# Performance work log

Measured on AMD Instinct MI355X. Metric: run time of the kernel, lower is better.

Reference implementation:

```python
import jax, jax.numpy as jnp
import numpy as np

B, N, D = 32, 2048, 512

def setup_inputs() -> dict:
    key = jax.random.key(0)
    k1, k2, k3, k4 = jax.random.split(key, 4)
    return {
        "src": jax.random.normal(k1, (B, N, 3), dtype=jnp.float32),
        "tgt": jax.random.normal(k2, (B, N, 3), dtype=jnp.float32),
        "src_embed": jax.random.normal(k3, (B, N, D), dtype=jnp.float32),
        "tgt_embed": jax.random.normal(k4, (B, N, D), dtype=jnp.float32),
    }

def reference(src, tgt, src_embed, tgt_embed):
    # src, tgt: (B, N, 3); src_embed, tgt_embed: (B, N, D)
    d_k = jnp.asarray(src_embed.shape[-1], dtype=src_embed.dtype)
    # attention scores (B, N_src, N_tgt), softmax over tgt points
    scores = jnp.einsum('bnd,bmd->bnm', src_embed, tgt_embed) / jnp.sqrt(d_k)
    pointer = jax.nn.softmax(scores, axis=2)
    # matched = tgt^T @ pointer^T -> (B, 3, N_src)
    matched = jnp.einsum('bmc,bnm->bcn', tgt, pointer)
    src_t = jnp.transpose(src, (0, 2, 1))  # (B, 3, N)
    src_cent = jnp.mean(src_t, axis=2, keepdims=True)        # (B, 3, 1)
    matched_cent = jnp.mean(matched, axis=2, keepdims=True)  # (B, 3, 1)
    src_demean = src_t - src_cent
    matched_demean = matched - matched_cent
    # cross-covariance H: (B, 3, 3)
    H = jnp.einsum('bcn,bdn->bcd', src_demean, matched_demean)
    U, _, Vh = jnp.linalg.svd(H, full_matrices=False)  # square 3x3: reduced == full
    V = jnp.transpose(Vh, (0, 2, 1))
    R = jnp.matmul(V, jnp.transpose(U, (0, 2, 1)))
    det = jnp.linalg.det(R)
    identity = jnp.eye(3, dtype=R.dtype)
    reflect = jnp.diag(jnp.array([1.0, 1.0, -1.0], dtype=R.dtype))
    refl = jnp.where((det >= 0)[:, None, None], identity, reflect)
    R = jnp.matmul(refl, R)
    t = jnp.matmul(-R, src_cent) + matched_cent  # (B, 3, 1)
    t = jnp.transpose(t, (0, 2, 1))              # (B, 1, 3)
    return (R, t)
```

## Files before the change

### kernel.cpp

```cpp
#include <hip/hip_runtime.h>
#include <hip/hip_fp16.h>
#include <math.h>

#define B_ 32
#define N_ 2048
#define D_ 512
#define NT 256

typedef __attribute__((ext_vector_type(8))) _Float16 f16x8;
typedef __attribute__((ext_vector_type(8))) short s16x8;
typedef __attribute__((ext_vector_type(4))) float f32x4;
typedef __attribute__((ext_vector_type(4))) unsigned int u32x4;

__device__ inline unsigned packh2(float lo, float hi) {
    __half l = __float2half_rn(lo), h = __float2half_rn(hi);
    return (unsigned)__half_as_ushort(l) | ((unsigned)__half_as_ushort(h) << 16);
}
__device__ inline unsigned f2bf(float x) {
    unsigned u = __float_as_uint(x);
    return (u + 0x7FFFu + ((u >> 16) & 1u)) >> 16;
}
__device__ inline float bf2f(unsigned h) { return __uint_as_float(h << 16); }

__global__ __launch_bounds__(256) void prepass_kernel(
    const float* __restrict__ te, u32x4* __restrict__ kp)
{
    const int idx = blockIdx.x * 256 + threadIdx.x;
    const int b   = idx >> 17;
    const int r17 = idx & 131071;
    const int mt  = r17 >> 13;
    const int kt  = (r17 >> 9) & 15;
    const int o16 = r17 & 511;
    const int r   = o16 >> 2;
    const int s   = o16 & 3;
    const int lg  = s ^ ((r >> 1) & 3);
    const float* src = te + (((size_t)b * N_ + mt * 128 + r) * D_ + kt * 32 + lg * 8);
    const float4 f0 = *(const float4*)src;
    const float4 f1 = *(const float4*)(src + 4);
    u32x4 u;
    u[0] = packh2(f0.x, f0.y);
    u[1] = packh2(f0.z, f0.w);
    u[2] = packh2(f1.x, f1.y);
    u[3] = packh2(f1.z, f1.w);
    kp[idx] = u;
}

__global__ __launch_bounds__(NT, 2) void attn_pipe_kernel(
    const float* __restrict__ src, const float* __restrict__ tgt,
    const float* __restrict__ src_embed, const u32x4* __restrict__ kp,
    float* __restrict__ partials)
{
    __shared__ f16x8 ring[4][512];
    __shared__ float4 Ts4[N_];
    __shared__ double red[4][15];

    const int tid  = threadIdx.x;
    const int wv   = tid >> 6;
    const int lane = tid & 63;
    const int lr   = lane & 15;
    const int lg   = lane >> 4;
    const int sxb  = (lg ^ ((lr >> 1) & 3)) << 4;
    char* ringB = (char*)&ring[0][0];

    const int xcd  = blockIdx.x & 7;
    const int idx  = blockIdx.x >> 3;
    const int b    = xcd * 4 + (idx >> 4);
    const int msl  = idx & 15;
    const int n0   = msl * 128;
    const int pblk = b * 16 + msl;

    const float QSC = 0.044194173824159216f * 1.4426950408889634f;
    f16x8 Qr[2][16];
#pragma unroll
    for (int qf = 0; qf < 2; ++qf) {
        const int qrow = n0 + wv * 32 + qf * 16 + lr;
        const float* qp = src_embed + ((size_t)b * N_ + qrow) * D_ + lg * 8;
#pragma unroll
        for (int s = 0; s < 16; ++s) {
            const float4 f0 = *(const float4*)(qp + s * 32);
            const float4 f1 = *(const float4*)(qp + s * 32 + 4);
            u32x4 u;
            u[0] = packh2(f0.x * QSC, f0.y * QSC);
            u[1] = packh2(f0.z * QSC, f0.w * QSC);
            u[2] = packh2(f1.x * QSC, f1.y * QSC);
            u[3] = packh2(f1.z * QSC, f1.w * QSC);
            Qr[qf][s] = __builtin_bit_cast(f16x8, u);
        }
    }
    {
        const float* tb = tgt + (size_t)b * N_ * 3;
#pragma unroll
        for (int i = 0; i < 8; ++i) {
            const int r = tid + i * 256;
            Ts4[r] = make_float4(tb[r * 3], tb[r * 3 + 1], tb[r * 3 + 2], 0.f);
        }
    }
    __syncthreads();

#define STAGE(mc_, kt_, slot_) do {                                            \
    const u32x4* _g = kp + ((((size_t)b * 16 + (mc_)) * 16 + (kt_)) << 9);     \
    __builtin_amdgcn_global_load_lds(                                          \
        (const __attribute__((address_space(1))) void*)(_g + tid),             \
        (__attribute__((address_space(3))) void*)(&ring[slot_][wv * 64]),      \
        16, 0, 0);                                                             \
    __builtin_amdgcn_global_load_lds(                                          \
        (const __attribute__((address_space(1))) void*)(_g + 256 + tid),       \
        (__attribute__((address_space(3))) void*)(&ring[slot_][256 + wv * 64]),\
        16, 0, 0);                                                             \
} while (0)

    STAGE(0, 0, 0);
    STAGE(0, 1, 1);
    STAGE(0, 2, 2);

    float m_s[2] = {-1e30f, -1e30f}, l_s[2] = {0.f, 0.f};
    float axs[2] = {0.f, 0.f}, ays[2] = {0.f, 0.f}, azs[2] = {0.f, 0.f};

    for (int mc = 0; mc < 16; ++mc) {
        f32x4 acc0[8], acc1[8];
#pragma unroll
        for (int nf = 0; nf < 8; ++nf) {
            acc0[nf] = (f32x4){0.f, 0.f, 0.f, 0.f};
            acc1[nf] = (f32x4){0.f, 0.f, 0.f, 0.f};
        }

#pragma unroll
        for (int kt = 0; kt < 16; ++kt) {
            const int t = (mc << 4) + kt;
            if (mc == 15 && kt >= 14) {
                asm volatile("s_waitcnt vmcnt(0)" ::: "memory");
            } else {
                asm volatile("s_waitcnt vmcnt(4)" ::: "memory");
            }
            __builtin_amdgcn_s_barrier();
            if (t <= 252) {
                const int tn = t + 3;
                STAGE(tn >> 4, tn & 15, tn & 3);
            }
            const char* abase = ringB + ((t & 3) << 13) + lr * 64 + sxb;
#pragma unroll
            for (int nf = 0; nf < 8; ++nf) {
                const f16x8 a = *(const f16x8*)(abase + nf * 1024);
                acc0[nf] = __builtin_amdgcn_mfma_f32_16x16x32_f16(a, Qr[0][kt], acc0[nf], 0, 0, 0);
                acc1[nf] = __builtin_amdgcn_mfma_f32_16x16x32_f16(a, Qr[1][kt], acc1[nf], 0, 0, 0);
            }
        }

        const float4* Ts = &Ts4[mc * 128];
        float mx0 = -1e30f, mx1 = -1e30f;
#pragma unroll
        for (int nf = 0; nf < 8; ++nf)
#pragma unroll
            for (int r4 = 0; r4 < 4; ++r4) {
                mx0 = fmaxf(mx0, acc0[nf][r4]);
                mx1 = fmaxf(mx1, acc1[nf][r4]);
            }
        mx0 = fmaxf(mx0, __shfl_xor(mx0, 16)); mx0 = fmaxf(mx0, __shfl_xor(mx0, 32));
        mx1 = fmaxf(mx1, __shfl_xor(mx1, 16)); mx1 = fmaxf(mx1, __shfl_xor(mx1, 32));
        const float mn0 = fmaxf(m_s[0], mx0), mn1 = fmaxf(m_s[1], mx1);
        const float c0 = exp2f(m_s[0] - mn0), c1 = exp2f(m_s[1] - mn1);
        l_s[0] *= c0; axs[0] *= c0; ays[0] *= c0; azs[0] *= c0; m_s[0] = mn0;
        l_s[1] *= c1; axs[1] *= c1; ays[1] *= c1; azs[1] *= c1; m_s[1] = mn1;
        float l0 = 0.f, x0 = 0.f, y0 = 0.f, z0 = 0.f;
        float l1 = 0.f, x1 = 0.f, y1 = 0.f, z1 = 0.f;
#pragma unroll
        for (int nf = 0; nf < 8; ++nf)
#pragma unroll
            for (int r4 = 0; r4 < 4; ++r4) {
                const float4 tv = Ts[nf * 16 + lg * 4 + r4];
                const float p0 = exp2f(acc0[nf][r4] - mn0);
                const float p1 = exp2f(acc1[nf][r4] - mn1);
                l0 += p0; x0 = fmaf(p0, tv.x, x0); y0 = fmaf(p0, tv.y, y0); z0 = fmaf(p0, tv.z, z0);
                l1 += p1; x1 = fmaf(p1, tv.x, x1); y1 = fmaf(p1, tv.y, y1); z1 = fmaf(p1, tv.z, z1);
            }
        l_s[0] += l0; axs[0] += x0; ays[0] += y0; azs[0] += z0;
        l_s[1] += l1; axs[1] += x1; ays[1] += y1; azs[1] += z1;
    }
#undef STAGE

    double dl[15];
#pragma unroll
    for (int i = 0; i < 15; ++i) dl[i] = 0.0;
#pragma unroll
    for (int qf = 0; qf < 2; ++qf) {
        float lt = l_s[qf], x = axs[qf], y = ays[qf], z = azs[qf];
        lt += __shfl_xor(lt, 16); lt += __shfl_xor(lt, 32);
        x  += __shfl_xor(x, 16);  x  += __shfl_xor(x, 32);
        y  += __shfl_xor(y, 16);  y  += __shfl_xor(y, 32);
        z  += __shfl_xor(z, 16);  z  += __shfl_xor(z, 32);
        if (lg == 0) {
            const int qrow = n0 + wv * 32 + qf * 16 + lr;
            const float* sp = src + ((size_t)b * N_ + qrow) * 3;
            const double inv = 1.0 / (double)lt;
            const double m0d = (double)x * inv, m1d = (double)y * inv, m2d = (double)z * inv;
            const double s0 = sp[0], s1 = sp[1], s2 = sp[2];
            dl[0] += s0;  dl[1] += s1;  dl[2] += s2;
            dl[3] += m0d; dl[4] += m1d; dl[5] += m2d;
            dl[6]  += s0 * m0d; dl[7]  += s0 * m1d; dl[8]  += s0 * m2d;
            dl[9]  += s1 * m0d; dl[10] += s1 * m1d; dl[11] += s1 * m2d;
            dl[12] += s2 * m0d; dl[13] += s2 * m1d; dl[14] += s2 * m2d;
        }
    }
#pragma unroll
    for (int i = 0; i < 15; ++i) {
        double v = dl[i];
        for (int off = 1; off < 64; off <<= 1) v += __shfl_xor(v, off);
        dl[i] = v;
    }
    if (lane == 0) {
#pragma unroll
        for (int i = 0; i < 15; ++i) red[wv][i] = dl[i];
    }
    __syncthreads();
    if (tid < 15) {
        double sum = 0.0;
        for (int w = 0; w < 4; ++w) sum += red[w][tid];
        partials[(size_t)pblk * 15 + tid] = (float)sum;
    }
}

__global__ __launch_bounds__(256, 2) void attn_v2_kernel(
    const float* __restrict__ src, const float* __restrict__ tgt,
    const float* __restrict__ src_embed, const float* __restrict__ tgt_embed,
    float* __restrict__ partials)
{
    __shared__ short Khi_s[128 * 64];
    __shared__ short Klo_s[128 * 64];
    __shared__ float4 Ts4[128];
    __shared__ double red[64][15];

    char* KhiB = (char*)Khi_s;
    char* KloB = (char*)Klo_s;

    const int w    = blockIdx.x;
    const int xcd  = w & 7;
    const int idx  = w >> 3;
    const int b    = xcd * 4 + (idx >> 5);
    const int n0   = (idx & 31) * 64;
    const int blk  = b * 32 + (idx & 31);

    const int tid  = threadIdx.x;
    const int wv   = tid >> 6;
    const int lane = tid & 63;
    const int lr   = lane & 15;
    const int lg   = lane >> 4;
    const unsigned swl = (unsigned)((lr & 7) << 4);

    const float scale = 0.044194173824159216f;
    const float* kbase = tgt_embed + (size_t)b * N_ * D_;

    const int qrow = n0 + wv * 16 + lr;
    const float* qp = src_embed + ((size_t)b * N_ + qrow) * D_ + lg * 8;
    s16x8 qhi[16], qlo[16];
#pragma unroll
    for (int s = 0; s < 16; ++s) {
        const float4 f0 = *reinterpret_cast<const float4*>(qp + s * 32);
        const float4 f1 = *reinterpret_cast<const float4*>(qp + s * 32 + 4);
        const float x[8] = {f0.x, f0.y, f0.z, f0.w, f1.x, f1.y, f1.z, f1.w};
#pragma unroll
        for (int i = 0; i < 8; ++i) {
            const float v = x[i] * scale;
            const unsigned h = f2bf(v);
            qhi[s][i] = (short)h;
            qlo[s][i] = (short)f2bf(v - bf2f(h));
        }
    }

    float m_run = -1e30f, l_run = 0.f, a0 = 0.f, a1 = 0.f, a2 = 0.f;
    const int srow = tid >> 1;
    const int shalf = tid & 1;
    const unsigned swr = (unsigned)((srow & 7) << 4);

    for (int m0 = 0; m0 < N_; m0 += 128) {
        f32x4 acc[8];
#pragma unroll
        for (int nf = 0; nf < 8; ++nf) acc[nf] = (f32x4){0.f, 0.f, 0.f, 0.f};

#pragma unroll
        for (int kt = 0; kt < 8; ++kt) {
            __syncthreads();
            {
                const float* gp = kbase + (size_t)(m0 + srow) * D_ + kt * 64 + shalf * 32;
#pragma unroll
                for (int grp = 0; grp < 4; ++grp) {
                    const float4 fa = *reinterpret_cast<const float4*>(gp + grp * 8);
                    const float4 fb = *reinterpret_cast<const float4*>(gp + grp * 8 + 4);
                    const float x[8] = {fa.x, fa.y, fa.z, fa.w, fb.x, fb.y, fb.z, fb.w};
                    s16x8 hi, lo;
#pragma unroll
                    for (int i = 0; i < 8; ++i) {
                        const unsigned h = f2bf(x[i]);
                        hi[i] = (short)h;
                        lo[i] = (short)f2bf(x[i] - bf2f(h));
                    }
                    const unsigned off = (unsigned)srow * 128u +
                        (((unsigned)(shalf * 64 + grp * 16)) ^ swr);
                    *reinterpret_cast<s16x8*>(KhiB + off) = hi;
                    *reinterpret_cast<s16x8*>(KloB + off) = lo;
                }
                if (kt == 0 && tid < 128) {
                    const float* tp = tgt + ((size_t)b * N_ + m0 + tid) * 3;
                    Ts4[tid] = make_float4(tp[0], tp[1], tp[2], 0.f);
                }
            }
            __syncthreads();
#pragma unroll
            for (int ks = 0; ks < 2; ++ks) {
                const int s = kt * 2 + ks;
                const unsigned kb = ((unsigned)(lg * 16 + ks * 64)) ^ swl;
#pragma unroll
                for (int nf = 0; nf < 8; ++nf) {
                    const unsigned off = (unsigned)(nf * 16 + lr) * 128u + kb;
                    const s16x8 ah = *reinterpret_cast<const s16x8*>(KhiB + off);
                    const s16x8 al = *reinterpret_cast<const s16x8*>(KloB + off);
                    acc[nf] = __builtin_amdgcn_mfma_f32_16x16x32_bf16(ah, qhi[s], acc[nf], 0, 0, 0);
                    acc[nf] = __builtin_amdgcn_mfma_f32_16x16x32_bf16(al, qhi[s], acc[nf], 0, 0, 0);
                    acc[nf] = __builtin_amdgcn_mfma_f32_16x16x32_bf16(ah, qlo[s], acc[nf], 0, 0, 0);
                }
            }
        }

        float mx = -1e30f;
#pragma unroll
        for (int nf = 0; nf < 8; ++nf)
#pragma unroll
            for (int r = 0; r < 4; ++r) mx = fmaxf(mx, acc[nf][r]);
        mx = fmaxf(mx, __shfl_xor(mx, 16));
        mx = fmaxf(mx, __shfl_xor(mx, 32));

        const float mnew = fmaxf(m_run, mx);
        const float corr = __expf(m_run - mnew);
        l_run *= corr; a0 *= corr; a1 *= corr; a2 *= corr;

        float ps = 0.f, p0 = 0.f, p1 = 0.f, p2 = 0.f;
#pragma unroll
        for (int nf = 0; nf < 8; ++nf)
#pragma unroll
            for (int r = 0; r < 4; ++r) {
                const float p = __expf(acc[nf][r] - mnew);
                const int n = nf * 16 + lg * 4 + r;
                const float4 tv = Ts4[n];
                ps += p;
                p0 = fmaf(p, tv.x, p0);
                p1 = fmaf(p, tv.y, p1);
                p2 = fmaf(p, tv.z, p2);
            }
        l_run += ps; a0 += p0; a1 += p1; a2 += p2;
        m_run = mnew;
    }

    l_run += __shfl_xor(l_run, 16); l_run += __shfl_xor(l_run, 32);
    a0 += __shfl_xor(a0, 16); a0 += __shfl_xor(a0, 32);
    a1 += __shfl_xor(a1, 16); a1 += __shfl_xor(a1, 32);
    a2 += __shfl_xor(a2, 16); a2 += __shfl_xor(a2, 32);

    __syncthreads();
    if (lg == 0) {
        const float inv = 1.0f / l_run;
        const double mx0 = (double)(a0 * inv);
        const double mx1 = (double)(a1 * inv);
        const double mx2 = (double)(a2 * inv);
        const float* sp = src + ((size_t)b * N_ + qrow) * 3;
        const double s0 = sp[0], s1 = sp[1], s2 = sp[2];
        double* rp = red[wv * 16 + lr];
        rp[0] = s0;  rp[1] = s1;  rp[2] = s2;
        rp[3] = mx0; rp[4] = mx1; rp[5] = mx2;
        rp[6]  = s0 * mx0; rp[7]  = s0 * mx1; rp[8]  = s0 * mx2;
        rp[9]  = s1 * mx0; rp[10] = s1 * mx1; rp[11] = s1 * mx2;
        rp[12] = s2 * mx0; rp[13] = s2 * mx1; rp[14] = s2 * mx2;
    }
    __syncthreads();
    if (tid < 15) {
        double sum = 0.0;
        for (int j = 0; j < 64; ++j) sum += red[j][tid];
        partials[(size_t)blk * 15 + tid] = (float)sum;
    }
}

__global__ void kabsch_kernel(const float* __restrict__ partials,
                              float* __restrict__ out, int nbb)
{
    const int b = threadIdx.x;
    if (b >= B_) return;

    double acc[15];
#pragma unroll
    for (int i = 0; i < 15; ++i) acc[i] = 0.0;
    for (int rb = 0; rb < nbb; ++rb) {
        const float* p = partials + ((size_t)b * nbb + rb) * 15;
#pragma unroll
        for (int i = 0; i < 15; ++i) acc[i] += (double)p[i];
    }

    const double invN = 1.0 / (double)N_;
    const double S[3] = {acc[0], acc[1], acc[2]};
    const double M[3] = {acc[3], acc[4], acc[5]};
    double H[3][3];
    for (int c = 0; c < 3; ++c)
        for (int d = 0; d < 3; ++d)
            H[c][d] = acc[6 + c * 3 + d] - S[c] * M[d] * invN;

    double A[3][3];
    for (int i = 0; i < 3; ++i)
        for (int j = 0; j < 3; ++j)
            A[i][j] = H[0][i] * H[0][j] + H[1][i] * H[1][j] + H[2][i] * H[2][j];

    double V[3][3] = {{1, 0, 0}, {0, 1, 0}, {0, 0, 1}};
    const int PQ[3][2] = {{0, 1}, {0, 2}, {1, 2}};
    for (int sweep = 0; sweep < 20; ++sweep) {
        const double off = fabs(A[0][1]) + fabs(A[0][2]) + fabs(A[1][2]);
        if (off < 1e-24) break;
        for (int pi = 0; pi < 3; ++pi) {
            const int p = PQ[pi][0], q = PQ[pi][1], rr = 3 - p - q;
            const double apq = A[p][q];
            if (fabs(apq) < 1e-300) continue;
            const double theta = (A[q][q] - A[p][p]) / (2.0 * apq);
            const double tt = (theta >= 0.0 ? 1.0 : -1.0) /
                              (fabs(theta) + sqrt(1.0 + theta * theta));
            const double c = 1.0 / sqrt(1.0 + tt * tt);
            const double sn = tt * c;
            const double app = A[p][p], aqq = A[q][q];
            const double arp = A[rr][p], arq = A[rr][q];
            A[p][p] = app - tt * apq;
            A[q][q] = aqq + tt * apq;
            A[p][q] = A[q][p] = 0.0;
            A[rr][p] = A[p][rr] = c * arp - sn * arq;
            A[rr][q] = A[q][rr] = sn * arp + c * arq;
            for (int k = 0; k < 3; ++k) {
                const double vkp = V[k][p], vkq = V[k][q];
                V[k][p] = c * vkp - sn * vkq;
                V[k][q] = sn * vkp + c * vkq;
            }
        }
    }

    double R[3][3] = {{0, 0, 0}, {0, 0, 0}, {0, 0, 0}};
    for (int i = 0; i < 3; ++i) {
        const double lam = A[i][i];
        const double sig = sqrt(lam > 0.0 ? lam : 0.0);
        const double inv = 1.0 / (sig > 1e-30 ? sig : 1e-30);
        double wv[3];
        for (int c = 0; c < 3; ++c)
            wv[c] = H[c][0] * V[0][i] + H[c][1] * V[1][i] + H[c][2] * V[2][i];
        for (int r = 0; r < 3; ++r)
            for (int c = 0; c < 3; ++c)
                R[r][c] += V[r][i] * wv[c] * inv;
    }

    const double det =
        R[0][0] * (R[1][1] * R[2][2] - R[1][2] * R[2][1]) -
        R[0][1] * (R[1][0] * R[2][2] - R[1][2] * R[2][0]) +
        R[0][2] * (R[1][0] * R[2][1] - R[1][1] * R[2][0]);
    if (det < 0.0) {
        R[2][0] = -R[2][0]; R[2][1] = -R[2][1]; R[2][2] = -R[2][2];
    }

    double t[3];
    for (int c = 0; c < 3; ++c)
        t[c] = M[c] * invN -
               (R[c][0] * S[0] + R[c][1] * S[1] + R[c][2] * S[2]) * invN;

    for (int r = 0; r < 3; ++r)
        for (int c = 0; c < 3; ++c)
            out[(size_t)b * 9 + r * 3 + c] = (float)R[r][c];
    for (int c = 0; c < 3; ++c)
        out[(size_t)B_ * 9 + (size_t)b * 3 + c] = (float)t[c];
}

extern "C" void kernel_launch(void* const* d_in, const int* in_sizes, int n_in,
                              void* d_out, int out_size, void* d_ws, size_t ws_size,
                              hipStream_t stream) {
    const float* src = (const float*)d_in[0];
    const float* tgt = (const float*)d_in[1];
    const float* se  = (const float*)d_in[2];
    const float* te  = (const float*)d_in[3];
    float* out = (float*)d_out;

    const size_t KP_OFF = 32768;
    const size_t need = KP_OFF + (size_t)B_ * N_ * D_ * 2;

    if (ws_size >= need) {
        u32x4* kp = (u32x4*)((char*)d_ws + KP_OFF);
        prepass_kernel<<<dim3(16384), dim3(256), 0, stream>>>(te, kp);
        attn_pipe_kernel<<<dim3(512), dim3(NT), 0, stream>>>(
            src, tgt, se, kp, (float*)d_ws);
        kabsch_kernel<<<dim3(1), dim3(64), 0, stream>>>((float*)d_ws, out, 16);
    } else {
        attn_v2_kernel<<<dim3(1024), dim3(256), 0, stream>>>(
            src, tgt, se, te, (float*)d_ws);
        kabsch_kernel<<<dim3(1), dim3(64), 0, stream>>>((float*)d_ws, out, 32);
    }
}
```

Baseline: 227.1 us.

## Double-buffer four-tile K groups with one barrier per group

```diff
diff --git a/kernel.cpp b/kernel.cpp
--- a/kernel.cpp
+++ b/kernel.cpp
@@ -45,13 +45,13 @@
     kp[idx] = u;
 }
 
-__global__ __launch_bounds__(NT, 2) void attn_pipe_kernel(
+__global__ __launch_bounds__(NT, 2) void attn_db_kernel(
     const float* __restrict__ src, const float* __restrict__ tgt,
     const float* __restrict__ src_embed, const u32x4* __restrict__ kp,
     float* __restrict__ partials)
 {
-    __shared__ f16x8 ring[4][512];
-    __shared__ float4 Ts4[N_];
+    __shared__ f16x8 Kbuf[2][4][512];
+    __shared__ float4 TsB[2][128];
     __shared__ double red[4][15];
 
     const int tid  = threadIdx.x;
@@ -60,7 +60,7 @@
     const int lr   = lane & 15;
     const int lg   = lane >> 4;
     const int sxb  = (lg ^ ((lr >> 1) & 3)) << 4;
-    char* ringB = (char*)&ring[0][0];
+    char* KbufB = (char*)&Kbuf[0][0][0];
 
     const int xcd  = blockIdx.x & 7;
     const int idx  = blockIdx.x >> 3;
@@ -87,96 +87,112 @@
             Qr[qf][s] = __builtin_bit_cast(f16x8, u);
         }
     }
-    {
-        const float* tb = tgt + (size_t)b * N_ * 3;
-#pragma unroll
-        for (int i = 0; i < 8; ++i) {
-            const int r = tid + i * 256;
-            Ts4[r] = make_float4(tb[r * 3], tb[r * 3 + 1], tb[r * 3 + 2], 0.f);
-        }
-    }
-    __syncthreads();
-
-#define STAGE(mc_, kt_, slot_) do {                                            \
-    const u32x4* _g = kp + ((((size_t)b * 16 + (mc_)) * 16 + (kt_)) << 9);     \
+    if (tid < 128) {
+        const float* tp = tgt + ((size_t)b * N_ + tid) * 3;
+        TsB[0][tid] = make_float4(tp[0], tp[1], tp[2], 0.f);
+    }
+
+#define STAGE_TILE(t_, half_, ti_) do {                                        \
+    const u32x4* _g = kp +                                                     \
+        ((((size_t)b * 16 + ((t_) >> 4)) * 16 + ((t_) & 15)) << 9);            \
     __builtin_amdgcn_global_load_lds(                                          \
         (const __attribute__((address_space(1))) void*)(_g + tid),             \
-        (__attribute__((address_space(3))) void*)(&ring[slot_][wv * 64]),      \
+        (__attribute__((address_space(3))) void*)(&Kbuf[half_][ti_][wv * 64]), \
         16, 0, 0);                                                             \
     __builtin_amdgcn_global_load_lds(                                          \
         (const __attribute__((address_space(1))) void*)(_g + 256 + tid),       \
-        (__attribute__((address_space(3))) void*)(&ring[slot_][256 + wv * 64]),\
+        (__attribute__((address_space(3))) void*)(&Kbuf[half_][ti_][256 + wv * 64]),\
         16, 0, 0);                                                             \
 } while (0)
 
-    STAGE(0, 0, 0);
-    STAGE(0, 1, 1);
-    STAGE(0, 2, 2);
+#define STAGE_GROUP(gi_, half_) do {                                           \
+    STAGE_TILE(4 * (gi_) + 0, half_, 0);                                       \
+    STAGE_TILE(4 * (gi_) + 1, half_, 1);                                       \
+    STAGE_TILE(4 * (gi_) + 2, half_, 2);                                       \
+    STAGE_TILE(4 * (gi_) + 3, half_, 3);                                       \
+} while (0)
+
+    STAGE_GROUP(0, 0);
 
     float m_s[2] = {-1e30f, -1e30f}, l_s[2] = {0.f, 0.f};
     float axs[2] = {0.f, 0.f}, ays[2] = {0.f, 0.f}, azs[2] = {0.f, 0.f};
 
-    for (int mc = 0; mc < 16; ++mc) {
-        f32x4 acc0[8], acc1[8];
-#pragma unroll
-        for (int nf = 0; nf < 8; ++nf) {
-            acc0[nf] = (f32x4){0.f, 0.f, 0.f, 0.f};
-            acc1[nf] = (f32x4){0.f, 0.f, 0.f, 0.f};
+    f32x4 acc0[8], acc1[8];
+
+    for (int g4 = 0; g4 < 16; ++g4) {
+#pragma unroll
+        for (int gm = 0; gm < 4; ++gm) {
+            const int g = (g4 << 2) | gm;
+            __syncthreads();
+            if (g < 63) {
+                const int gn = g + 1;
+                STAGE_GROUP(gn, gn & 1);
+            }
+            float tv0 = 0.f, tv1 = 0.f, tv2 = 0.f;
+            const bool pf = (gm == 3) && (g4 < 15) && (tid < 128);
+            if (pf) {
+                const float* tp = tgt + ((size_t)b * N_ + (g4 + 1) * 128 + tid) * 3;
+                tv0 = tp[0]; tv1 = tp[1]; tv2 = tp[2];
+            }
+            if (gm == 0) {
+#pragma unroll
+                for (int nf = 0; nf < 8; ++nf) {
+                    acc0[nf] = (f32x4){0.f, 0.f, 0.f, 0.f};
+                    acc1[nf] = (f32x4){0.f, 0.f, 0.f, 0.f};
+                }
+            }
+            __builtin_amdgcn_s_setprio(1);
+#pragma unroll
+            for (int ti = 0; ti < 4; ++ti) {
+                const int kt = (gm << 2) | ti;
+                const char* abase = KbufB + ((g & 1) << 15) + (ti << 13)
+                                  + lr * 64 + sxb;
+#pragma unroll
+                for (int nf = 0; nf < 8; ++nf) {
+                    const f16x8 a = *(const f16x8*)(abase + nf * 1024);
+                    acc0[nf] = __builtin_amdgcn_mfma_f32_16x16x32_f16(a, Qr[0][kt], acc0[nf], 0, 0, 0);
+                    acc1[nf] = __builtin_amdgcn_mfma_f32_16x16x32_f16(a, Qr[1][kt], acc1[nf], 0, 0, 0);
+                }
+            }
+            __builtin_amdgcn_s_setprio(0);
+            if (pf)
+                TsB[(g4 + 1) & 1][tid] = make_float4(tv0, tv1, tv2, 0.f);
+
+            if (gm == 3) {
+                const float4* Ts = &TsB[g4 & 1][0];
+                float mx0 = -1e30f, mx1 = -1e30f;
+#pragma unroll
+                for (int nf = 0; nf < 8; ++nf)
+#pragma unroll
+                    for (int r4 = 0; r4 < 4; ++r4) {
+                        mx0 = fmaxf(mx0, acc0[nf][r4]);
+                        mx1 = fmaxf(mx1, acc1[nf][r4]);
+                    }
+                mx0 = fmaxf(mx0, __shfl_xor(mx0, 16)); mx0 = fmaxf(mx0, __shfl_xor(mx0, 32));
+                mx1 = fmaxf(mx1, __shfl_xor(mx1, 16)); mx1 = fmaxf(mx1, __shfl_xor(mx1, 32));
+                const float mn0 = fmaxf(m_s[0], mx0), mn1 = fmaxf(m_s[1], mx1);
+                const float c0 = exp2f(m_s[0] - mn0), c1 = exp2f(m_s[1] - mn1);
+                l_s[0] *= c0; axs[0] *= c0; ays[0] *= c0; azs[0] *= c0; m_s[0] = mn0;
+                l_s[1] *= c1; axs[1] *= c1; ays[1] *= c1; azs[1] *= c1; m_s[1] = mn1;
+                float l0 = 0.f, x0 = 0.f, y0 = 0.f, z0 = 0.f;
+                float l1 = 0.f, x1 = 0.f, y1 = 0.f, z1 = 0.f;
+#pragma unroll
+                for (int nf = 0; nf < 8; ++nf)
+#pragma unroll
+                    for (int r4 = 0; r4 < 4; ++r4) {
+                        const float4 tv = Ts[nf * 16 + lg * 4 + r4];
+                        const float p0 = exp2f(acc0[nf][r4] - mn0);
+                        const float p1 = exp2f(acc1[nf][r4] - mn1);
+                        l0 += p0; x0 = fmaf(p0, tv.x, x0); y0 = fmaf(p0, tv.y, y0); z0 = fmaf(p0, tv.z, z0);
+                        l1 += p1; x1 = fmaf(p1, tv.x, x1); y1 = fmaf(p1, tv.y, y1); z1 = fmaf(p1, tv.z, z1);
+                    }
+                l_s[0] += l0; axs[0] += x0; ays[0] += y0; azs[0] += z0;
+                l_s[1] += l1; axs[1] += x1; ays[1] += y1; azs[1] += z1;
+            }
         }
-
-#pragma unroll
-        for (int kt = 0; kt < 16; ++kt) {
-            const int t = (mc << 4) + kt;
-            if (mc == 15 && kt >= 14) {
-                asm volatile("s_waitcnt vmcnt(0)" ::: "memory");
-            } else {
-                asm volatile("s_waitcnt vmcnt(4)" ::: "memory");
-            }
-            __builtin_amdgcn_s_barrier();
-            if (t <= 252) {
-                const int tn = t + 3;
-                STAGE(tn >> 4, tn & 15, tn & 3);
-            }
-            const char* abase = ringB + ((t & 3) << 13) + lr * 64 + sxb;
-#pragma unroll
-            for (int nf = 0; nf < 8; ++nf) {
-                const f16x8 a = *(const f16x8*)(abase + nf * 1024);
-                acc0[nf] = __builtin_amdgcn_mfma_f32_16x16x32_f16(a, Qr[0][kt], acc0[nf], 0, 0, 0);
-                acc1[nf] = __builtin_amdgcn_mfma_f32_16x16x32_f16(a, Qr[1][kt], acc1[nf], 0, 0, 0);
-            }
-        }
-
-        const float4* Ts = &Ts4[mc * 128];
-        float mx0 = -1e30f, mx1 = -1e30f;
-#pragma unroll
-        for (int nf = 0; nf < 8; ++nf)
-#pragma unroll
-            for (int r4 = 0; r4 < 4; ++r4) {
-                mx0 = fmaxf(mx0, acc0[nf][r4]);
-                mx1 = fmaxf(mx1, acc1[nf][r4]);
-            }
-        mx0 = fmaxf(mx0, __shfl_xor(mx0, 16)); mx0 = fmaxf(mx0, __shfl_xor(mx0, 32));
-        mx1 = fmaxf(mx1, __shfl_xor(mx1, 16)); mx1 = fmaxf(mx1, __shfl_xor(mx1, 32));
-        const float mn0 = fmaxf(m_s[0], mx0), mn1 = fmaxf(m_s[1], mx1);
-        const float c0 = exp2f(m_s[0] - mn0), c1 = exp2f(m_s[1] - mn1);
-        l_s[0] *= c0; axs[0] *= c0; ays[0] *= c0; azs[0] *= c0; m_s[0] = mn0;
-        l_s[1] *= c1; axs[1] *= c1; ays[1] *= c1; azs[1] *= c1; m_s[1] = mn1;
-        float l0 = 0.f, x0 = 0.f, y0 = 0.f, z0 = 0.f;
-        float l1 = 0.f, x1 = 0.f, y1 = 0.f, z1 = 0.f;
-#pragma unroll
-        for (int nf = 0; nf < 8; ++nf)
-#pragma unroll
-            for (int r4 = 0; r4 < 4; ++r4) {
-                const float4 tv = Ts[nf * 16 + lg * 4 + r4];
-                const float p0 = exp2f(acc0[nf][r4] - mn0);
-                const float p1 = exp2f(acc1[nf][r4] - mn1);
-                l0 += p0; x0 = fmaf(p0, tv.x, x0); y0 = fmaf(p0, tv.y, y0); z0 = fmaf(p0, tv.z, z0);
-                l1 += p1; x1 = fmaf(p1, tv.x, x1); y1 = fmaf(p1, tv.y, y1); z1 = fmaf(p1, tv.z, z1);
-            }
-        l_s[0] += l0; axs[0] += x0; ays[0] += y0; azs[0] += z0;
-        l_s[1] += l1; axs[1] += x1; ays[1] += y1; azs[1] += z1;
-    }
-#undef STAGE
+    }
+#undef STAGE_GROUP
+#undef STAGE_TILE
 
     double dl[15];
 #pragma unroll
@@ -482,7 +498,7 @@
     if (ws_size >= need) {
         u32x4* kp = (u32x4*)((char*)d_ws + KP_OFF);
         prepass_kernel<<<dim3(16384), dim3(256), 0, stream>>>(te, kp);
-        attn_pipe_kernel<<<dim3(512), dim3(NT), 0, stream>>>(
+        attn_db_kernel<<<dim3(512), dim3(NT), 0, stream>>>(
             src, tgt, se, kp, (float*)d_ws);
         kabsch_kernel<<<dim3(1), dim3(64), 0, stream>>>((float*)d_ws, out, 16);
     } else {
```

New measurement: 226.5 us (median of 2 runs). Within noise of the previous version (-0.3%).

## Give each wave a private K ring, dropping block-wide barriers in the attention loop

Applied to the files above, without the earlier changes.

```diff
diff --git a/kernel.cpp b/kernel.cpp
--- a/kernel.cpp
+++ b/kernel.cpp
@@ -9,6 +9,7 @@
 
 typedef __attribute__((ext_vector_type(8))) _Float16 f16x8;
 typedef __attribute__((ext_vector_type(8))) short s16x8;
+typedef __attribute__((ext_vector_type(4))) short s16x4;
 typedef __attribute__((ext_vector_type(4))) float f32x4;
 typedef __attribute__((ext_vector_type(4))) unsigned int u32x4;
 
@@ -45,13 +46,15 @@
     kp[idx] = u;
 }
 
-__global__ __launch_bounds__(NT, 2) void attn_pipe_kernel(
+__global__ __launch_bounds__(NT, 2) void attn_async_kernel(
     const float* __restrict__ src, const float* __restrict__ tgt,
     const float* __restrict__ src_embed, const u32x4* __restrict__ kp,
     float* __restrict__ partials)
 {
-    __shared__ f16x8 ring[4][512];
-    __shared__ float4 Ts4[N_];
+    __shared__ f16x8 ring[4][2][512];
+    __shared__ unsigned short Tsx[N_];
+    __shared__ unsigned short Tsy[N_];
+    __shared__ unsigned short Tsz[N_];
     __shared__ double red[4][15];
 
     const int tid  = threadIdx.x;
@@ -60,7 +63,7 @@
     const int lr   = lane & 15;
     const int lg   = lane >> 4;
     const int sxb  = (lg ^ ((lr >> 1) & 3)) << 4;
-    char* ringB = (char*)&ring[0][0];
+    char* ringB = (char*)&ring[0][0][0];
 
     const int xcd  = blockIdx.x & 7;
     const int idx  = blockIdx.x >> 3;
@@ -88,35 +91,50 @@
         }
     }
     {
-        const float* tb = tgt + (size_t)b * N_ * 3;
+        const float* tb = tgt + (size_t)b * N_ * 3 + (size_t)tid * 24;
+        float f[24];
+#pragma unroll
+        for (int i = 0; i < 6; ++i) {
+            const float4 v = *(const float4*)(tb + i * 4);
+            f[i * 4 + 0] = v.x; f[i * 4 + 1] = v.y;
+            f[i * 4 + 2] = v.z; f[i * 4 + 3] = v.w;
+        }
+        s16x8 hx, hy, hz;
 #pragma unroll
         for (int i = 0; i < 8; ++i) {
-            const int r = tid + i * 256;
-            Ts4[r] = make_float4(tb[r * 3], tb[r * 3 + 1], tb[r * 3 + 2], 0.f);
-        }
+            hx[i] = (short)__half_as_ushort(__float2half_rn(f[3 * i + 0]));
+            hy[i] = (short)__half_as_ushort(__float2half_rn(f[3 * i + 1]));
+            hz[i] = (short)__half_as_ushort(__float2half_rn(f[3 * i + 2]));
+        }
+        *(s16x8*)&Tsx[tid * 8] = hx;
+        *(s16x8*)&Tsy[tid * 8] = hy;
+        *(s16x8*)&Tsz[tid * 8] = hz;
     }
     __syncthreads();
 
-#define STAGE(mc_, kt_, slot_) do {                                            \
-    const u32x4* _g = kp + ((((size_t)b * 16 + (mc_)) * 16 + (kt_)) << 9);     \
-    __builtin_amdgcn_global_load_lds(                                          \
-        (const __attribute__((address_space(1))) void*)(_g + tid),             \
-        (__attribute__((address_space(3))) void*)(&ring[slot_][wv * 64]),      \
-        16, 0, 0);                                                             \
-    __builtin_amdgcn_global_load_lds(                                          \
-        (const __attribute__((address_space(1))) void*)(_g + 256 + tid),       \
-        (__attribute__((address_space(3))) void*)(&ring[slot_][256 + wv * 64]),\
-        16, 0, 0);                                                             \
+#define WSTAGE(mc_, kt_, slot_) do {                                           \
+    const u32x4* _g = kp +                                                     \
+        ((((size_t)b * 16 + (mc_)) * 16 + (kt_)) << 9) + lane;                 \
+    _Pragma("unroll")                                                          \
+    for (int _i = 0; _i < 8; ++_i)                                             \
+        __builtin_amdgcn_global_load_lds(                                      \
+            (const __attribute__((address_space(1))) void*)(_g + _i * 64),     \
+            (__attribute__((address_space(3))) void*)(&ring[wv][slot_][_i * 64]),\
+            16, 0, 0);                                                         \
 } while (0)
 
-    STAGE(0, 0, 0);
-    STAGE(0, 1, 1);
-    STAGE(0, 2, 2);
+    const int wv4 = wv << 2;
+    const int mc0 = wv4 & 15;
+    WSTAGE(mc0, 0, 0);
+    WSTAGE(mc0, 1, 1);
 
     float m_s[2] = {-1e30f, -1e30f}, l_s[2] = {0.f, 0.f};
     float axs[2] = {0.f, 0.f}, ays[2] = {0.f, 0.f}, azs[2] = {0.f, 0.f};
 
-    for (int mc = 0; mc < 16; ++mc) {
+    for (int j = 0; j < 16; ++j) {
+        const int mc  = (wv4 + j) & 15;
+        const int mcn = (mc + 1) & 15;
+
         f32x4 acc0[8], acc1[8];
 #pragma unroll
         for (int nf = 0; nf < 8; ++nf) {
@@ -126,27 +144,35 @@
 
 #pragma unroll
         for (int kt = 0; kt < 16; ++kt) {
-            const int t = (mc << 4) + kt;
-            if (mc == 15 && kt >= 14) {
-                asm volatile("s_waitcnt vmcnt(0)" ::: "memory");
+            if (kt == 15) {
+                if (j == 15) { asm volatile("s_waitcnt vmcnt(0)" ::: "memory"); }
+                else         { asm volatile("s_waitcnt vmcnt(8)" ::: "memory"); }
             } else {
-                asm volatile("s_waitcnt vmcnt(4)" ::: "memory");
-            }
-            __builtin_amdgcn_s_barrier();
-            if (t <= 252) {
-                const int tn = t + 3;
-                STAGE(tn >> 4, tn & 15, tn & 3);
-            }
-            const char* abase = ringB + ((t & 3) << 13) + lr * 64 + sxb;
+                asm volatile("s_waitcnt vmcnt(8)" ::: "memory");
+            }
+            const char* abase = ringB + (wv << 14) + ((kt & 1) << 13)
+                              + lr * 64 + sxb;
+            f16x8 a[8];
+#pragma unroll
+            for (int nf = 0; nf < 8; ++nf)
+                a[nf] = *(const f16x8*)(abase + nf * 1024);
+            __builtin_amdgcn_s_setprio(1);
 #pragma unroll
             for (int nf = 0; nf < 8; ++nf) {
-                const f16x8 a = *(const f16x8*)(abase + nf * 1024);
-                acc0[nf] = __builtin_amdgcn_mfma_f32_16x16x32_f16(a, Qr[0][kt], acc0[nf], 0, 0, 0);
-                acc1[nf] = __builtin_amdgcn_mfma_f32_16x16x32_f16(a, Qr[1][kt], acc1[nf], 0, 0, 0);
-            }
-        }
-
-        const float4* Ts = &Ts4[mc * 128];
+                acc0[nf] = __builtin_amdgcn_mfma_f32_16x16x32_f16(a[nf], Qr[0][kt], acc0[nf], 0, 0, 0);
+                acc1[nf] = __builtin_amdgcn_mfma_f32_16x16x32_f16(a[nf], Qr[1][kt], acc1[nf], 0, 0, 0);
+            }
+            __builtin_amdgcn_s_setprio(0);
+            asm volatile("s_waitcnt lgkmcnt(0)" ::: "memory");
+            if (kt <= 13) {
+                WSTAGE(mc, kt + 2, kt & 1);
+            } else if (kt == 14) {
+                if (j < 15) WSTAGE(mcn, 0, 0);
+            } else {
+                if (j < 15) WSTAGE(mcn, 1, 1);
+            }
+        }
+
         float mx0 = -1e30f, mx1 = -1e30f;
 #pragma unroll
         for (int nf = 0; nf < 8; ++nf)
@@ -163,20 +189,28 @@
         l_s[1] *= c1; axs[1] *= c1; ays[1] *= c1; azs[1] *= c1; m_s[1] = mn1;
         float l0 = 0.f, x0 = 0.f, y0 = 0.f, z0 = 0.f;
         float l1 = 0.f, x1 = 0.f, y1 = 0.f, z1 = 0.f;
-#pragma unroll
-        for (int nf = 0; nf < 8; ++nf)
+        const int tb0 = (mc << 7) + lg * 4;
+#pragma unroll
+        for (int nf = 0; nf < 8; ++nf) {
+            const int base = tb0 + nf * 16;
+            const s16x4 hx = *(const s16x4*)&Tsx[base];
+            const s16x4 hy = *(const s16x4*)&Tsy[base];
+            const s16x4 hz = *(const s16x4*)&Tsz[base];
 #pragma unroll
             for (int r4 = 0; r4 < 4; ++r4) {
-                const float4 tv = Ts[nf * 16 + lg * 4 + r4];
+                const float tx = __half2float(__ushort_as_half((unsigned short)hx[r4]));
+                const float ty = __half2float(__ushort_as_half((unsigned short)hy[r4]));
+                const float tz = __half2float(__ushort_as_half((unsigned short)hz[r4]));
                 const float p0 = exp2f(acc0[nf][r4] - mn0);
                 const float p1 = exp2f(acc1[nf][r4] - mn1);
-                l0 += p0; x0 = fmaf(p0, tv.x, x0); y0 = fmaf(p0, tv.y, y0); z0 = fmaf(p0, tv.z, z0);
-                l1 += p1; x1 = fmaf(p1, tv.x, x1); y1 = fmaf(p1, tv.y, y1); z1 = fmaf(p1, tv.z, z1);
-            }
+                l0 += p0; x0 = fmaf(p0, tx, x0); y0 = fmaf(p0, ty, y0); z0 = fmaf(p0, tz, z0);
+                l1 += p1; x1 = fmaf(p1, tx, x1); y1 = fmaf(p1, ty, y1); z1 = fmaf(p1, tz, z1);
+            }
+        }
         l_s[0] += l0; axs[0] += x0; ays[0] += y0; azs[0] += z0;
         l_s[1] += l1; axs[1] += x1; ays[1] += y1; azs[1] += z1;
     }
-#undef STAGE
+#undef WSTAGE
 
     double dl[15];
 #pragma unroll
@@ -482,7 +516,7 @@
     if (ws_size >= need) {
         u32x4* kp = (u32x4*)((char*)d_ws + KP_OFF);
         prepass_kernel<<<dim3(16384), dim3(256), 0, stream>>>(te, kp);
-        attn_pipe_kernel<<<dim3(512), dim3(NT), 0, stream>>>(
+        attn_async_kernel<<<dim3(512), dim3(NT), 0, stream>>>(
             src, tgt, se, kp, (float*)d_ws);
         kabsch_kernel<<<dim3(1), dim3(64), 0, stream>>>((float*)d_ws, out, 16);
     } else {
```

Result: slower. 297.3 us (+30.9%).

## Load key fragments directly from global memory instead of an LDS ring pipeline

Applied to the files above, without the earlier changes.

```diff
diff --git a/kernel.cpp b/kernel.cpp
--- a/kernel.cpp
+++ b/kernel.cpp
@@ -45,12 +45,11 @@
     kp[idx] = u;
 }
 
-__global__ __launch_bounds__(NT, 2) void attn_pipe_kernel(
+__global__ __launch_bounds__(NT, 2) void attn_stream_kernel(
     const float* __restrict__ src, const float* __restrict__ tgt,
     const float* __restrict__ src_embed, const u32x4* __restrict__ kp,
     float* __restrict__ partials)
 {
-    __shared__ f16x8 ring[4][512];
     __shared__ float4 Ts4[N_];
     __shared__ double red[4][15];
 
@@ -60,7 +59,6 @@
     const int lr   = lane & 15;
     const int lg   = lane >> 4;
     const int sxb  = (lg ^ ((lr >> 1) & 3)) << 4;
-    char* ringB = (char*)&ring[0][0];
 
     const int xcd  = blockIdx.x & 7;
     const int idx  = blockIdx.x >> 3;
@@ -68,6 +66,9 @@
     const int msl  = idx & 15;
     const int n0   = msl * 128;
     const int pblk = b * 16 + msl;
+
+    const int lo   = lr * 4 + (sxb >> 4);
+    const u32x4* kpb = kp + ((size_t)b << 12) * 32 + lo;
 
     const float QSC = 0.044194173824159216f * 1.4426950408889634f;
     f16x8 Qr[2][16];
@@ -97,26 +98,12 @@
     }
     __syncthreads();
 
-#define STAGE(mc_, kt_, slot_) do {                                            \
-    const u32x4* _g = kp + ((((size_t)b * 16 + (mc_)) * 16 + (kt_)) << 9);     \
-    __builtin_amdgcn_global_load_lds(                                          \
-        (const __attribute__((address_space(1))) void*)(_g + tid),             \
-        (__attribute__((address_space(3))) void*)(&ring[slot_][wv * 64]),      \
-        16, 0, 0);                                                             \
-    __builtin_amdgcn_global_load_lds(                                          \
-        (const __attribute__((address_space(1))) void*)(_g + 256 + tid),       \
-        (__attribute__((address_space(3))) void*)(&ring[slot_][256 + wv * 64]),\
-        16, 0, 0);                                                             \
-} while (0)
-
-    STAGE(0, 0, 0);
-    STAGE(0, 1, 1);
-    STAGE(0, 2, 2);
-
     float m_s[2] = {-1e30f, -1e30f}, l_s[2] = {0.f, 0.f};
     float axs[2] = {0.f, 0.f}, ays[2] = {0.f, 0.f}, azs[2] = {0.f, 0.f};
 
     for (int mc = 0; mc < 16; ++mc) {
+        const u32x4* tb = kpb + ((size_t)mc << 13);
+
         f32x4 acc0[8], acc1[8];
 #pragma unroll
         for (int nf = 0; nf < 8; ++nf) {
@@ -126,23 +113,14 @@
 
 #pragma unroll
         for (int kt = 0; kt < 16; ++kt) {
-            const int t = (mc << 4) + kt;
-            if (mc == 15 && kt >= 14) {
-                asm volatile("s_waitcnt vmcnt(0)" ::: "memory");
-            } else {
-                asm volatile("s_waitcnt vmcnt(4)" ::: "memory");
-            }
-            __builtin_amdgcn_s_barrier();
-            if (t <= 252) {
-                const int tn = t + 3;
-                STAGE(tn >> 4, tn & 15, tn & 3);
-            }
-            const char* abase = ringB + ((t & 3) << 13) + lr * 64 + sxb;
+            f16x8 a[8];
+#pragma unroll
+            for (int nf = 0; nf < 8; ++nf)
+                a[nf] = __builtin_bit_cast(f16x8, tb[(kt << 9) + nf * 64]);
 #pragma unroll
             for (int nf = 0; nf < 8; ++nf) {
-                const f16x8 a = *(const f16x8*)(abase + nf * 1024);
-                acc0[nf] = __builtin_amdgcn_mfma_f32_16x16x32_f16(a, Qr[0][kt], acc0[nf], 0, 0, 0);
-                acc1[nf] = __builtin_amdgcn_mfma_f32_16x16x32_f16(a, Qr[1][kt], acc1[nf], 0, 0, 0);
+                acc0[nf] = __builtin_amdgcn_mfma_f32_16x16x32_f16(a[nf], Qr[0][kt], acc0[nf], 0, 0, 0);
+                acc1[nf] = __builtin_amdgcn_mfma_f32_16x16x32_f16(a[nf], Qr[1][kt], acc1[nf], 0, 0, 0);
             }
         }
 
@@ -176,7 +154,6 @@
         l_s[0] += l0; axs[0] += x0; ays[0] += y0; azs[0] += z0;
         l_s[1] += l1; axs[1] += x1; ays[1] += y1; azs[1] += z1;
     }
-#undef STAGE
 
     double dl[15];
 #pragma unroll
@@ -482,7 +459,7 @@
     if (ws_size >= need) {
         u32x4* kp = (u32x4*)((char*)d_ws + KP_OFF);
         prepass_kernel<<<dim3(16384), dim3(256), 0, stream>>>(te, kp);
-        attn_pipe_kernel<<<dim3(512), dim3(NT), 0, stream>>>(
+        attn_stream_kernel<<<dim3(512), dim3(NT), 0, stream>>>(
             src, tgt, se, kp, (float*)d_ws);
         kabsch_kernel<<<dim3(1), dim3(64), 0, stream>>>((float*)d_ws, out, 16);
     } else {
```

Result: slower. 693.2 us (+205.3%).
